# Optimization experiments

Measured on AMD Instinct MI355X. Metric: run time of the kernel, lower is better.

Reference implementation:

```python
import jax, jax.numpy as jnp
import numpy as np

VOCAB = 32000; D_MODEL = 768; N_LAYERS = 4
D_STATE = 16; D_CONV = 4; EXPAND = 2
D_INNER = EXPAND * D_MODEL                 # 1536
DT_RANK = (D_MODEL + 15) // 16             # 48
BATCH = 2; SEQ = 1024


def setup_inputs():
    key = jax.random.key(0)
    ks = jax.random.split(key, 10)
    def nrm(k, shape, scale=0.02):
        return (jax.random.normal(k, shape) * scale).astype(jnp.float32)
    inp = {}
    inp['tokens'] = jax.random.randint(ks[0], (BATCH, SEQ), 0, VOCAB)
    inp['embedding'] = nrm(ks[1], (VOCAB, D_MODEL))
    inp['head_bias'] = jnp.zeros((VOCAB,), jnp.float32)
    inp['ln_g'] = jnp.ones((N_LAYERS, D_MODEL), jnp.float32)
    inp['ln_b'] = jnp.zeros((N_LAYERS, D_MODEL), jnp.float32)
    inp['W_in'] = nrm(ks[2], (N_LAYERS, 2 * D_INNER, D_MODEL))
    inp['conv_w'] = nrm(ks[3], (N_LAYERS, D_INNER, 1, D_CONV), 0.1)
    inp['conv_b'] = jnp.zeros((N_LAYERS, D_INNER), jnp.float32)
    inp['W_xproj'] = nrm(ks[4], (N_LAYERS, DT_RANK + 2 * D_STATE, D_INNER))
    inp['W_dt'] = nrm(ks[5], (N_LAYERS, D_INNER, DT_RANK), 0.1)
    inp['b_dt'] = nrm(ks[6], (N_LAYERS, D_INNER), 0.5)
    # S4D-real init: A_n = n for n in 1..d_state
    inp['A_log'] = jnp.broadcast_to(jnp.log(jnp.arange(1, D_STATE + 1, dtype=jnp.float32)), (N_LAYERS, D_INNER, D_STATE)).copy()
    inp['D_ssm'] = jnp.ones((N_LAYERS, D_INNER), jnp.float32)
    inp['W_out'] = nrm(ks[7], (N_LAYERS, D_MODEL, D_INNER))
    inp['norm_g'] = jnp.ones((D_MODEL,), jnp.float32)
    inp['norm_b'] = jnp.zeros((D_MODEL,), jnp.float32)
    return inp


def _ln(x, g, b):
    m = jnp.mean(x, axis=-1, keepdims=True)
    v = jnp.var(x, axis=-1, keepdims=True)
    return (x - m) * jax.lax.rsqrt(v + 1e-5) * g + b


def _mamba(x, W_in, conv_w, conv_b, W_xproj, W_dt, b_dt, A_log, D_ssm, W_out):
    # x: (S, B, D_MODEL)
    xz = jnp.einsum('sbd,ed->sbe', x, W_in)           # (S, B, 2*D_INNER)
    xc, z = jnp.split(xz, 2, axis=-1)
    # depthwise causal conv along sequence
    xt = jnp.transpose(xc, (1, 2, 0))                  # (B, C, S)
    xt = jax.lax.conv_general_dilated(xt, conv_w, (1,), [(D_CONV - 1, 0)],
                                      dimension_numbers=('NCH', 'OIH', 'NCH'),
                                      feature_group_count=D_INNER)
    xt = xt + conv_b[None, :, None]
    xc = jax.nn.silu(jnp.transpose(xt, (2, 0, 1)))     # (S, B, C)
    xdb = jnp.einsum('sbc,ec->sbe', xc, W_xproj)       # (S, B, DT_RANK+2N)
    dt_r = xdb[..., :DT_RANK]
    Bm = xdb[..., DT_RANK:DT_RANK + D_STATE]
    Cm = xdb[..., DT_RANK + D_STATE:]
    dt = jax.nn.softplus(jnp.einsum('sbr,cr->sbc', dt_r, W_dt) + b_dt)
    A = -jnp.exp(A_log)                                # (C, N)

    def step(h, t):
        dt_t, B_t, C_t, x_t = t                        # (B,C),(B,N),(B,N),(B,C)
        dA = jnp.exp(dt_t[..., None] * A)              # (B, C, N)
        h = h * dA + (dt_t * x_t)[..., None] * B_t[:, None, :]
        y = jnp.einsum('bcn,bn->bc', h, C_t)
        return h, y

    h0 = jnp.zeros((x.shape[1], D_INNER, D_STATE), x.dtype)
    _, ys = jax.lax.scan(step, h0, (dt, Bm, Cm, xc))   # ys: (S, B, C)
    y = (ys + D_ssm * xc) * jax.nn.silu(z)
    return jnp.einsum('sbc,dc->sbd', y, W_out)


def reference(tokens, embedding, head_bias, ln_g, ln_b, W_in, conv_w, conv_b, W_xproj, W_dt, b_dt, A_log, D_ssm, W_out, norm_g, norm_b):
    x = embedding[tokens.T]                            # (S, B, D)
    for i in range(N_LAYERS):
        x = x + _mamba(_ln(x, ln_g[i], ln_b[i]), W_in[i], conv_w[i], conv_b[i],
                       W_xproj[i], W_dt[i], b_dt[i], A_log[i], D_ssm[i], W_out[i])
    x = _ln(x, norm_g, norm_b)
    logits = jnp.einsum('sbd,vd->sbv', x, embedding) + head_bias  # tied head
    return jnp.transpose(logits, (1, 0, 2))            # (B, S, VOCAB)
```

## Files before the change

### kernel.cpp

```cpp
#include <hip/hip_runtime.h>
#include <hip/hip_bf16.h>
#include <cstdint>
#include <cstddef>

#define SEQ_LEN 1024
#define NBATCH  2
#define MROWS   2048
#define DMODEL  768
#define DINNER  1536
#define DTRANK  48
#define DSTATE  16
#define NLAYERS 4
#define NVOCAB  32000
#define XPROJ_N 80
#define NCHUNK  16
#define CHUNK   64
#define GROUPS  (NBATCH * DINNER)
#define SCANW   (GROUPS * DSTATE)
#define XSPLIT  8

typedef __attribute__((ext_vector_type(4))) float f32x4;
typedef __attribute__((ext_vector_type(8))) short s16x8;
using bf16 = __hip_bfloat16;

__device__ __forceinline__ float b2f(bf16 v){ return __bfloat162float(v); }
__device__ __forceinline__ bf16  f2b(float v){ return __float2bfloat16(v); }
__device__ __forceinline__ short f2bs(float v){
  return (short)__builtin_bit_cast(unsigned short, __float2bfloat16(v));
}

__device__ __forceinline__ void glds16(const ushort* g, ushort* l) {
  __builtin_amdgcn_global_load_lds(
      (const __attribute__((address_space(1))) void*)g,
      (__attribute__((address_space(3))) void*)l,
      16, 0, 0);
}

#define CVT_E0 6144000
#define CVT_E1 (CVT_E0 + 2359296)
#define CVT_E2 (CVT_E1 + 1179648)
#define CVT_E3 (CVT_E2 + 122880)
#define CVT_E4 (CVT_E3 + 73728)
__global__ __launch_bounds__(256) void k_cvt5(
    const float* __restrict__ s0, const float* __restrict__ s1,
    const float* __restrict__ s2, const float* __restrict__ s3,
    const float* __restrict__ s4,
    ushort* __restrict__ d0, ushort* __restrict__ d1,
    ushort* __restrict__ d2, ushort* __restrict__ d3,
    ushort* __restrict__ d4)
{
  int i = blockIdx.x * 256 + threadIdx.x;
  const float* s; ushort* d; int base;
  if      (i < CVT_E0) { s = s0; d = d0; base = 0; }
  else if (i < CVT_E1) { s = s1; d = d1; base = CVT_E0; }
  else if (i < CVT_E2) { s = s2; d = d2; base = CVT_E1; }
  else if (i < CVT_E3) { s = s3; d = d3; base = CVT_E2; }
  else if (i < CVT_E4) { s = s4; d = d4; base = CVT_E3; }
  else return;
  int li = i - base;
  f32x4 v = *(const f32x4*)(s + (size_t)li * 4);
  ushort4 o;
  o.x = (ushort)f2bs(v[0]); o.y = (ushort)f2bs(v[1]);
  o.z = (ushort)f2bs(v[2]); o.w = (ushort)f2bs(v[3]);
  *(ushort4*)(d + (size_t)li * 4) = o;
}

__global__ __launch_bounds__(256) void k_xsum(const float* __restrict__ p,
    ushort* __restrict__ out, int n4) {
  int i = blockIdx.x * 256 + threadIdx.x;
  if (i >= n4) return;
  f32x4 s = {};
#pragma unroll
  for (int z = 0; z < XSPLIT; z++) {
    f32x4 v = *(const f32x4*)(p + (size_t)z * (MROWS * XPROJ_N) + (size_t)i * 4);
    s[0] += v[0]; s[1] += v[1]; s[2] += v[2]; s[3] += v[3];
  }
  ushort4 o;
  o.x = (ushort)f2bs(s[0]); o.y = (ushort)f2bs(s[1]);
  o.z = (ushort)f2bs(s[2]); o.w = (ushort)f2bs(s[3]);
  *(ushort4*)(out + (size_t)i * 4) = o;
}

__device__ __forceinline__ void ln_rows(const float v0[3], int t,
    const float* __restrict__ g, const float* __restrict__ b,
    bf16* __restrict__ outrow) {
  float s = 0.f, s2 = 0.f;
#pragma unroll
  for (int j = 0; j < 3; j++) { s += v0[j]; s2 += v0[j] * v0[j]; }
#pragma unroll
  for (int o = 32; o >= 1; o >>= 1) { s += __shfl_xor(s, o); s2 += __shfl_xor(s2, o); }
  __shared__ float red[8];
  int wave = t >> 6;
  if ((t & 63) == 0) { red[wave] = s; red[4 + wave] = s2; }
  __syncthreads();
  s  = red[0] + red[1] + red[2] + red[3];
  s2 = red[4] + red[5] + red[6] + red[7];
  float mean = s * (1.f / DMODEL);
  float var  = s2 * (1.f / DMODEL) - mean * mean;
  float rstd = rsqrtf(var + 1e-5f);
#pragma unroll
  for (int j = 0; j < 3; j++) {
    int d = t + j * 256;
    outrow[d] = f2b((v0[j] - mean) * rstd * g[d] + b[d]);
  }
}

__global__ __launch_bounds__(256) void k_ln(const float* __restrict__ x,
    bf16* __restrict__ out, const float* __restrict__ g, const float* __restrict__ b) {
  int m = blockIdx.x;
  const float* row = x + (size_t)m * DMODEL;
  int t = threadIdx.x;
  float v0[3];
#pragma unroll
  for (int j = 0; j < 3; j++) v0[j] = row[t + j * 256];
  ln_rows(v0, t, g, b, out + (size_t)m * DMODEL);
}

__global__ __launch_bounds__(256) void k_embed_ln(const int* __restrict__ tok,
    const float* __restrict__ emb, float* __restrict__ x,
    bf16* __restrict__ out, const float* __restrict__ g, const float* __restrict__ b) {
  int m = blockIdx.x;
  const float* row = emb + (size_t)tok[m] * DMODEL;
  int t = threadIdx.x;
  float v0[3];
#pragma unroll
  for (int j = 0; j < 3; j++) {
    v0[j] = row[t + j * 256];
    x[(size_t)m * DMODEL + t + j * 256] = v0[j];
  }
  ln_rows(v0, t, g, b, out + (size_t)m * DMODEL);
}

template<bool HAS_BIAS, int OMODE>
__global__ __launch_bounds__(512, 4) void k_gemm128(
    const ushort* __restrict__ A, int lda,
    const ushort* __restrict__ B, int ldb,
    void* __restrict__ C, int ldc,
    const float* __restrict__ bias,
    int M, int N, int K)
{
  __shared__ ushort As[2][128 * 32];
  __shared__ ushort Bs[2][128 * 32];
  const int t = threadIdx.x;
  const int lane = t & 63;
  const int wave = t >> 6;
  const int tile_m = blockIdx.x * 128;
  const int tile_n = blockIdx.y * 128;
  const int kper = K / gridDim.z;
  const int kb = blockIdx.z * kper;
  const int ke = kb + kper;
  const int wr = (wave >> 1) * 32;
  const int wc = (wave & 1) * 64;

  f32x4 acc[2][4] = {};

  const int sr = wave * 16 + (lane >> 2);
  const int sc = (lane & 3) * 8;
  const ushort* gA = A + (size_t)(tile_m + sr) * lda + sc + kb;
  const ushort* gB = B + (size_t)(tile_n + sr) * ldb + sc + kb;

  const int fr = lane & 15;
  const int kk = (lane >> 4) * 8;

  auto stage = [&](int bb) {
    glds16(gA, &As[bb][wave * 512]);
    glds16(gB, &Bs[bb][wave * 512]);
    gA += 32; gB += 32;
  };

  stage(0);
  int cur = 0;

  for (int k0 = kb; k0 < ke; k0 += 32) {
    if (k0 + 32 < ke) {
      stage(cur ^ 1);
      asm volatile("s_waitcnt vmcnt(2)" ::: "memory");
    } else {
      asm volatile("s_waitcnt vmcnt(0)" ::: "memory");
    }
    __builtin_amdgcn_s_barrier();

    s16x8 a[2], b[4];
#pragma unroll
    for (int m = 0; m < 2; m++)
      a[m] = *(const s16x8*)&As[cur][(wr + m * 16 + fr) * 32 + kk];
#pragma unroll
    for (int n = 0; n < 4; n++)
      b[n] = *(const s16x8*)&Bs[cur][(wc + n * 16 + fr) * 32 + kk];
#pragma unroll
    for (int m = 0; m < 2; m++)
#pragma unroll
      for (int n = 0; n < 4; n++)
        acc[m][n] = __builtin_amdgcn_mfma_f32_16x16x32_bf16(a[m], b[n], acc[m][n], 0, 0, 0);

    __builtin_amdgcn_s_barrier();
    cur ^= 1;
  }

  const int rq = (lane >> 4) * 4;
#pragma unroll
  for (int m = 0; m < 2; m++)
#pragma unroll
    for (int n = 0; n < 4; n++) {
      int colg = tile_n + wc + n * 16 + fr;
      float bv = HAS_BIAS ? bias[colg] : 0.f;
#pragma unroll
      for (int r = 0; r < 4; r++) {
        int rowg = tile_m + wr + m * 16 + rq + r;
        size_t idx = (size_t)rowg * ldc + colg;
        float v = acc[m][n][r] + bv;
        if constexpr (OMODE == 0) ((float*)C)[idx] = v;
        else if constexpr (OMODE == 1) atomicAdd((float*)C + idx, v);
        else ((bf16*)C)[idx] = f2b(v);
      }
    }
}

template<int MODE>
__global__ __launch_bounds__(256) void k_gemm(
    const ushort* __restrict__ A, int lda,
    const ushort* __restrict__ W, int ldw,
    void* __restrict__ Cout, int ldc,
    int M, int N, int K,
    const float* __restrict__ bias,
    const bf16* __restrict__ xcb,
    bf16* __restrict__ dtxp)
{
  __shared__ ushort As[64][40];
  __shared__ ushort Ws[64][40];
  const int tile_m = blockIdx.x * 64;
  const int tile_n = blockIdx.y * 64;
  const int t = threadIdx.x;
  const int lane = t & 63;
  const int wave = t >> 6;
  const int wr = (wave >> 1) * 32;
  const int wc = (wave & 1) * 32;
  f32x4 acc[2][2] = {};

  const int kper = ((K + gridDim.z - 1) / gridDim.z + 31) & ~31;
  const int kb = blockIdx.z * kper;
  int ke = kb + kper; if (ke > K) ke = K;

  const int srow = t >> 2;
  const int scol = (t & 3) * 8;

  for (int k0 = kb; k0 < ke; k0 += 32) {
    {
      int gm = tile_m + srow, gk = k0 + scol;
      s16x8 v = {};
      if (gm < M) {
        if (gk + 8 <= K) v = *(const s16x8*)(A + (size_t)gm * lda + gk);
        else {
#pragma unroll
          for (int j = 0; j < 8; j++) if (gk + j < K) v[j] = (short)A[(size_t)gm * lda + gk + j];
        }
      }
      *(s16x8*)&As[srow][scol] = v;
    }
    {
      int gn = tile_n + srow, gk = k0 + scol;
      s16x8 v = {};
      if (gn < N) {
        if (gk + 8 <= K) v = *(const s16x8*)(W + (size_t)gn * ldw + gk);
        else {
#pragma unroll
          for (int j = 0; j < 8; j++) if (gk + j < K) v[j] = (short)W[(size_t)gn * ldw + gk + j];
        }
      }
      *(s16x8*)&Ws[srow][scol] = v;
    }
    __syncthreads();
    const int kk = (lane >> 4) * 8;
    const int fr = lane & 15;
    s16x8 a0 = *(const s16x8*)&As[wr + fr][kk];
    s16x8 a1 = *(const s16x8*)&As[wr + 16 + fr][kk];
    s16x8 b0 = *(const s16x8*)&Ws[wc + fr][kk];
    s16x8 b1 = *(const s16x8*)&Ws[wc + 16 + fr][kk];
    acc[0][0] = __builtin_amdgcn_mfma_f32_16x16x32_bf16(a0, b0, acc[0][0], 0, 0, 0);
    acc[0][1] = __builtin_amdgcn_mfma_f32_16x16x32_bf16(a0, b1, acc[0][1], 0, 0, 0);
    acc[1][0] = __builtin_amdgcn_mfma_f32_16x16x32_bf16(a1, b0, acc[1][0], 0, 0, 0);
    acc[1][1] = __builtin_amdgcn_mfma_f32_16x16x32_bf16(a1, b1, acc[1][1], 0, 0, 0);
    __syncthreads();
  }

  const int fr = lane & 15;
  const int rq = (lane >> 4) * 4;
#pragma unroll
  for (int i = 0; i < 2; i++)
#pragma unroll
    for (int j = 0; j < 2; j++) {
      int colg = tile_n + wc + j * 16 + fr;
#pragma unroll
      for (int r = 0; r < 4; r++) {
        int rowg = tile_m + wr + i * 16 + rq + r;
        if (rowg < M && colg < N) {
          float v = acc[i][j][r];
          size_t idx = (size_t)rowg * ldc + colg;
          if constexpr (MODE == 0) {
            ((bf16*)Cout)[idx] = f2b(v);
          } else if constexpr (MODE == 2) {
            v += bias[colg];
            float sp = (v > 20.f) ? v : log1pf(__expf(v));
            ((float*)Cout)[idx] = sp;
            dtxp[idx] = f2b(sp * b2f(xcb[idx]));
          } else {
            ((float*)Cout)[(size_t)blockIdx.z * (MROWS * XPROJ_N) + idx] = v;
          }
        }
      }
    }
}

__global__ __launch_bounds__(256) void k_conv(const bf16* __restrict__ xz,
    const float* __restrict__ w, const float* __restrict__ cb,
    bf16* __restrict__ xcb) {
  int id = blockIdx.x * 256 + threadIdx.x;
  int m = id / DINNER, c = id - m * DINNER;
  int s = m & (SEQ_LEN - 1);
  float acc = cb[c];
#pragma unroll
  for (int k = 0; k < 4; k++) {
    int sp = s - 3 + k;
    if (sp >= 0) acc += w[c * 4 + k] * b2f(xz[(size_t)(m - 3 + k) * (2 * DINNER) + c]);
  }
  float sil = acc / (1.f + __expf(-acc));
  xcb[id] = f2b(sil);
}

__global__ __launch_bounds__(256) void k_scan1(const float* __restrict__ dt,
    const bf16* __restrict__ dtx, const bf16* __restrict__ xdb,
    const float* __restrict__ A_log, float* __restrict__ aprod,
    float* __restrict__ hend) {
  int gid = blockIdx.x * 256 + threadIdx.x;
  int n  = gid & 15;
  int t2 = gid >> 4;
  int j  = t2 / GROUPS;
  int cb = t2 - j * GROUPS;
  int c  = cb % DINNER;
  int b  = cb / DINNER;
  float Acn = -__expf(A_log[c * DSTATE + n]);
  float h = 0.f, ap = 1.f;
  int mbase = b * SEQ_LEN + j * CHUNK;
#pragma unroll 4
  for (int s = 0; s < CHUNK; s++) {
    int m = mbase + s;
    float dtv = dt[(size_t)m * DINNER + c];
    float dxv = b2f(dtx[(size_t)m * DINNER + c]);
    float Bv  = b2f(xdb[(size_t)m * XPROJ_N + DTRANK + n]);
    float dA  = __expf(dtv * Acn);
    h = h * dA + dxv * Bv;
    ap *= dA;
  }
  aprod[gid] = ap;
  hend[gid]  = h;
}

__global__ __launch_bounds__(256) void k_scan2(const float* __restrict__ aprod,
    const float* __restrict__ hend, float* __restrict__ hin) {
  int idx = blockIdx.x * 256 + threadIdx.x;
  float h = 0.f;
#pragma unroll
  for (int j = 0; j < NCHUNK; j++) {
    hin[(size_t)j * SCANW + idx] = h;
    h = aprod[(size_t)j * SCANW + idx] * h + hend[(size_t)j * SCANW + idx];
  }
}

__global__ __launch_bounds__(256) void k_scan3(const float* __restrict__ dt,
    const bf16* __restrict__ dtx, const bf16* __restrict__ xdb,
    const float* __restrict__ A_log, const float* __restrict__ hin,
    bf16* __restrict__ y) {
  int gid = blockIdx.x * 256 + threadIdx.x;
  int n  = gid & 15;
  int t2 = gid >> 4;
  int j  = t2 / GROUPS;
  int cb = t2 - j * GROUPS;
  int c  = cb % DINNER;
  int b  = cb / DINNER;
  float Acn = -__expf(A_log[c * DSTATE + n]);
  float h = hin[gid];
  int mbase = b * SEQ_LEN + j * CHUNK;
#pragma unroll 2
  for (int s = 0; s < CHUNK; s++) {
    int m = mbase + s;
    float dtv = dt[(size_t)m * DINNER + c];
    float dxv = b2f(dtx[(size_t)m * DINNER + c]);
    float Bv  = b2f(xdb[(size_t)m * XPROJ_N + DTRANK + n]);
    float Cv  = b2f(xdb[(size_t)m * XPROJ_N + DTRANK + DSTATE + n]);
    float dA  = __expf(dtv * Acn);
    h = h * dA + dxv * Bv;
    float p = h * Cv;
    p += __shfl_xor(p, 8);
    p += __shfl_xor(p, 4);
    p += __shfl_xor(p, 2);
    p += __shfl_xor(p, 1);
    if (n == 0) y[(size_t)m * DINNER + c] = f2b(p);
  }
}

__global__ __launch_bounds__(256) void k_ycomb(const bf16* __restrict__ y,
    const bf16* __restrict__ xcb, const bf16* __restrict__ xz,
    const float* __restrict__ D_ssm, bf16* __restrict__ ybf) {
  int id = blockIdx.x * 256 + threadIdx.x;
  int m = id / DINNER, c = id - m * DINNER;
  float z = b2f(xz[(size_t)m * (2 * DINNER) + DINNER + c]);
  float sil = z / (1.f + __expf(-z));
  float v = (b2f(y[id]) + D_ssm[c] * b2f(xcb[id])) * sil;
  ybf[id] = f2b(v);
}

extern "C" void kernel_launch(void* const* d_in, const int* in_sizes, int n_in,
                              void* d_out, int out_size, void* d_ws, size_t ws_size,
                              hipStream_t stream) {
  const int*   tokens    = (const int*)  d_in[0];
  const float* embedding = (const float*)d_in[1];
  const float* head_bias = (const float*)d_in[2];
  const float* ln_g      = (const float*)d_in[3];
  const float* ln_b      = (const float*)d_in[4];
  const float* W_in      = (const float*)d_in[5];
  const float* conv_w    = (const float*)d_in[6];
  const float* conv_b    = (const float*)d_in[7];
  const float* W_xproj   = (const float*)d_in[8];
  const float* W_dt      = (const float*)d_in[9];
  const float* b_dt      = (const float*)d_in[10];
  const float* A_log     = (const float*)d_in[11];
  const float* D_ssm     = (const float*)d_in[12];
  const float* W_out     = (const float*)d_in[13];
  const float* norm_g    = (const float*)d_in[14];
  const float* norm_b    = (const float*)d_in[15];
  float* out = (float*)d_out;

  char* ws = (char*)d_ws;
  size_t off = 0;
  auto alloc = [&](size_t bytes) -> char* {
    char* p = ws + off;
    off = (off + bytes + 255) & ~(size_t)255;
    return p;
  };
  float*  x     = (float*) alloc((size_t)MROWS * DMODEL * 4);
  bf16*   xln   = (bf16*)  alloc((size_t)MROWS * DMODEL * 2);
  bf16*   xz    = (bf16*)  alloc((size_t)MROWS * 2 * DINNER * 2);
  bf16*   xcb   = (bf16*)  alloc((size_t)MROWS * DINNER * 2);
  bf16*   xdb   = (bf16*)  alloc((size_t)MROWS * XPROJ_N * 2);
  float*  xdbp  = (float*) alloc((size_t)XSPLIT * MROWS * XPROJ_N * 4);
  float*  dtf   = (float*) alloc((size_t)MROWS * DINNER * 4);
  bf16*   dtx   = (bf16*)  alloc((size_t)MROWS * DINNER * 2);
  bf16*   yraw  = (bf16*)  alloc((size_t)MROWS * DINNER * 2);
  bf16*   ybf   = (bf16*)  alloc((size_t)MROWS * DINNER * 2);
  float*  aprod = (float*) alloc((size_t)SCANW * NCHUNK * 4);
  float*  hend  = (float*) alloc((size_t)SCANW * NCHUNK * 4);
  float*  hin   = (float*) alloc((size_t)SCANW * NCHUNK * 4);
  ushort* ebf   = (ushort*)alloc((size_t)NVOCAB * DMODEL * 2);
  ushort* winb  = (ushort*)alloc((size_t)NLAYERS * 2 * DINNER * DMODEL * 2);
  ushort* wxpb  = (ushort*)alloc((size_t)NLAYERS * XPROJ_N * DINNER * 2);
  ushort* wdtb  = (ushort*)alloc((size_t)NLAYERS * DINNER * DTRANK * 2);
  ushort* woutb = (ushort*)alloc((size_t)NLAYERS * DMODEL * DINNER * 2);
  (void)ws_size; (void)in_sizes; (void)n_in; (void)out_size;

  k_cvt5<<<(CVT_E4 + 255) / 256, 256, 0, stream>>>(
      embedding, W_in, W_out, W_xproj, W_dt,
      ebf, winb, woutb, wxpb, wdtb);

  k_embed_ln<<<MROWS, 256, 0, stream>>>(tokens, embedding, x, xln, ln_g, ln_b);

  const int XDBN4 = MROWS * XPROJ_N / 4;

  for (int L = 0; L < NLAYERS; L++) {
    if (L > 0)
      k_ln<<<MROWS, 256, 0, stream>>>(x, xln, ln_g + L * DMODEL, ln_b + L * DMODEL);

    k_gemm128<false, 2><<<dim3(MROWS / 128, (2 * DINNER) / 128), 512, 0, stream>>>(
        (const ushort*)xln, DMODEL,
        winb + (size_t)L * 2 * DINNER * DMODEL, DMODEL,
        (void*)xz, 2 * DINNER, nullptr, MROWS, 2 * DINNER, DMODEL);

    k_conv<<<MROWS * DINNER / 256, 256, 0, stream>>>(
        xz, conv_w + (size_t)L * DINNER * 4, conv_b + (size_t)L * DINNER, xcb);

    k_gemm<3><<<dim3(MROWS / 64, 2, XSPLIT), 256, 0, stream>>>(
        (const ushort*)xcb, DINNER,
        wxpb + (size_t)L * XPROJ_N * DINNER, DINNER,
        (void*)xdbp, XPROJ_N, MROWS, XPROJ_N, DINNER,
        nullptr, nullptr, nullptr);
    k_xsum<<<(XDBN4 + 255) / 256, 256, 0, stream>>>(xdbp, (ushort*)xdb, XDBN4);

    k_gemm<2><<<dim3(MROWS / 64, DINNER / 64), 256, 0, stream>>>(
        (const ushort*)xdb, XPROJ_N,
        wdtb + (size_t)L * DINNER * DTRANK, DTRANK,
        (void*)dtf, DINNER, MROWS, DINNER, DTRANK,
        b_dt + (size_t)L * DINNER, xcb, dtx);

    const float* Al = A_log + (size_t)L * DINNER * DSTATE;
    k_scan1<<<SCANW * NCHUNK / 256, 256, 0, stream>>>(dtf, dtx, xdb, Al, aprod, hend);
    k_scan2<<<SCANW / 256, 256, 0, stream>>>(aprod, hend, hin);
    k_scan3<<<SCANW * NCHUNK / 256, 256, 0, stream>>>(dtf, dtx, xdb, Al, hin, yraw);

    k_ycomb<<<MROWS * DINNER / 256, 256, 0, stream>>>(
        yraw, xcb, xz, D_ssm + (size_t)L * DINNER, ybf);

    k_gemm128<false, 1><<<dim3(MROWS / 128, DMODEL / 128, 4), 512, 0, stream>>>(
        (const ushort*)ybf, DINNER,
        woutb + (size_t)L * DMODEL * DINNER, DINNER,
        (void*)x, DMODEL, nullptr, MROWS, DMODEL, DINNER);
  }

  k_ln<<<MROWS, 256, 0, stream>>>(x, xln, norm_g, norm_b);

  k_gemm128<true, 0><<<dim3(MROWS / 128, NVOCAB / 128), 512, 0, stream>>>(
      (const ushort*)xln, DMODEL,
      ebf, DMODEL,
      out, NVOCAB, head_bias, MROWS, NVOCAB, DMODEL);
}
```

Before: 980.9 us.

## Fuse three-pass chunked scan into one kernel and enlarge LM-head GEMM tile

The chunked selective scan's three kernels (per-chunk reduce, cross-chunk prefix, per-chunk apply) become one kernel. Each block handles one (batch, channel) pair, and the cross-chunk carry is resolved in shared memory, so the aprod/hend/hin global buffers and two launches per layer go away. The scan inputs are also read twice within the same block, which may improve cache reuse. The LM-head GEMM moves to a new 256x128-tile kernel with double-buffered direct-to-LDS loads, meant to cut repeated embedding-matrix reads. The trade-off is higher register and LDS use per block, and a serial prefix over 16 chunks inside each block.

```diff
diff --git a/kernel.cpp b/kernel.cpp
--- a/kernel.cpp
+++ b/kernel.cpp
@@ -216,6 +216,86 @@
     }
 }
 
+template<bool HAS_BIAS>
+__global__ __launch_bounds__(512, 4) void k_gemmbig(
+    const ushort* __restrict__ A, int lda,
+    const ushort* __restrict__ B, int ldb,
+    float* __restrict__ C, int ldc,
+    const float* __restrict__ bias,
+    int M, int N, int K)
+{
+  __shared__ ushort As[2][256 * 32];
+  __shared__ ushort Bs[2][128 * 32];
+  const int t = threadIdx.x;
+  const int lane = t & 63;
+  const int wave = t >> 6;
+  const int tile_m = blockIdx.x * 256;
+  const int tile_n = blockIdx.y * 128;
+  const int wr = (wave >> 1) * 64;
+  const int wc = (wave & 1) * 64;
+
+  f32x4 acc[4][4] = {};
+
+  const int sr = wave * 16 + (lane >> 2);
+  const int sc = (lane & 3) * 8;
+  const ushort* gA0 = A + (size_t)(tile_m + sr) * lda + sc;
+  const ushort* gA1 = A + (size_t)(tile_m + 128 + sr) * lda + sc;
+  const ushort* gB  = B + (size_t)(tile_n + sr) * ldb + sc;
+
+  const int fr = lane & 15;
+  const int kk = (lane >> 4) * 8;
+
+  auto stage = [&](int bb) {
+    glds16(gA0, &As[bb][wave * 512]);
+    glds16(gA1, &As[bb][4096 + wave * 512]);
+    glds16(gB,  &Bs[bb][wave * 512]);
+    gA0 += 32; gA1 += 32; gB += 32;
+  };
+
+  stage(0);
+  int cur = 0;
+
+  for (int k0 = 0; k0 < K; k0 += 32) {
+    if (k0 + 32 < K) {
+      stage(cur ^ 1);
+      asm volatile("s_waitcnt vmcnt(3)" ::: "memory");
+    } else {
+      asm volatile("s_waitcnt vmcnt(0)" ::: "memory");
+    }
+    __builtin_amdgcn_s_barrier();
+
+    s16x8 a[4], b[4];
+#pragma unroll
+    for (int m = 0; m < 4; m++)
+      a[m] = *(const s16x8*)&As[cur][(wr + m * 16 + fr) * 32 + kk];
+#pragma unroll
+    for (int n = 0; n < 4; n++)
+      b[n] = *(const s16x8*)&Bs[cur][(wc + n * 16 + fr) * 32 + kk];
+#pragma unroll
+    for (int m = 0; m < 4; m++)
+#pragma unroll
+      for (int n = 0; n < 4; n++)
+        acc[m][n] = __builtin_amdgcn_mfma_f32_16x16x32_bf16(a[m], b[n], acc[m][n], 0, 0, 0);
+
+    __builtin_amdgcn_s_barrier();
+    cur ^= 1;
+  }
+
+  const int rq = (lane >> 4) * 4;
+#pragma unroll
+  for (int m = 0; m < 4; m++)
+#pragma unroll
+    for (int n = 0; n < 4; n++) {
+      int colg = tile_n + wc + n * 16 + fr;
+      float bv = HAS_BIAS ? bias[colg] : 0.f;
+#pragma unroll
+      for (int r = 0; r < 4; r++) {
+        int rowg = tile_m + wr + m * 16 + rq + r;
+        C[(size_t)rowg * ldc + colg] = acc[m][n][r] + bv;
+      }
+    }
+}
+
 template<int MODE>
 __global__ __launch_bounds__(256) void k_gemm(
     const ushort* __restrict__ A, int lda,
@@ -327,20 +407,17 @@
   xcb[id] = f2b(sil);
 }
 
-__global__ __launch_bounds__(256) void k_scan1(const float* __restrict__ dt,
+__global__ __launch_bounds__(256) void k_scan(const float* __restrict__ dt,
     const bf16* __restrict__ dtx, const bf16* __restrict__ xdb,
-    const float* __restrict__ A_log, float* __restrict__ aprod,
-    float* __restrict__ hend) {
-  int gid = blockIdx.x * 256 + threadIdx.x;
-  int n  = gid & 15;
-  int t2 = gid >> 4;
-  int j  = t2 / GROUPS;
-  int cb = t2 - j * GROUPS;
-  int c  = cb % DINNER;
-  int b  = cb / DINNER;
+    const float* __restrict__ A_log, bf16* __restrict__ y) {
+  int cb = blockIdx.x;
+  int c = cb % DINNER, b = cb / DINNER;
+  int t = threadIdx.x;
+  int n = t & 15, j = t >> 4;
   float Acn = -__expf(A_log[c * DSTATE + n]);
+  int mbase = b * SEQ_LEN + j * CHUNK;
+
   float h = 0.f, ap = 1.f;
-  int mbase = b * SEQ_LEN + j * CHUNK;
 #pragma unroll 4
   for (int s = 0; s < CHUNK; s++) {
     int m = mbase + s;
@@ -351,35 +428,23 @@
     h = h * dA + dxv * Bv;
     ap *= dA;
   }
-  aprod[gid] = ap;
-  hend[gid]  = h;
-}
-
-__global__ __launch_bounds__(256) void k_scan2(const float* __restrict__ aprod,
-    const float* __restrict__ hend, float* __restrict__ hin) {
-  int idx = blockIdx.x * 256 + threadIdx.x;
-  float h = 0.f;
-#pragma unroll
-  for (int j = 0; j < NCHUNK; j++) {
-    hin[(size_t)j * SCANW + idx] = h;
-    h = aprod[(size_t)j * SCANW + idx] * h + hend[(size_t)j * SCANW + idx];
-  }
-}
-
-__global__ __launch_bounds__(256) void k_scan3(const float* __restrict__ dt,
-    const bf16* __restrict__ dtx, const bf16* __restrict__ xdb,
-    const float* __restrict__ A_log, const float* __restrict__ hin,
-    bf16* __restrict__ y) {
-  int gid = blockIdx.x * 256 + threadIdx.x;
-  int n  = gid & 15;
-  int t2 = gid >> 4;
-  int j  = t2 / GROUPS;
-  int cb = t2 - j * GROUPS;
-  int c  = cb % DINNER;
-  int b  = cb / DINNER;
-  float Acn = -__expf(A_log[c * DSTATE + n]);
-  float h = hin[gid];
-  int mbase = b * SEQ_LEN + j * CHUNK;
+
+  __shared__ float Ap[NCHUNK][DSTATE + 1];
+  __shared__ float He[NCHUNK][DSTATE + 1];
+  __shared__ float Hin[NCHUNK][DSTATE + 1];
+  Ap[j][n] = ap; He[j][n] = h;
+  __syncthreads();
+  if (t < DSTATE) {
+    float hh = 0.f;
+#pragma unroll
+    for (int jj = 0; jj < NCHUNK; jj++) {
+      Hin[jj][t] = hh;
+      hh = Ap[jj][t] * hh + He[jj][t];
+    }
+  }
+  __syncthreads();
+
+  h = Hin[j][n];
 #pragma unroll 2
   for (int s = 0; s < CHUNK; s++) {
     int m = mbase + s;
@@ -447,9 +512,6 @@
   bf16*   dtx   = (bf16*)  alloc((size_t)MROWS * DINNER * 2);
   bf16*   yraw  = (bf16*)  alloc((size_t)MROWS * DINNER * 2);
   bf16*   ybf   = (bf16*)  alloc((size_t)MROWS * DINNER * 2);
-  float*  aprod = (float*) alloc((size_t)SCANW * NCHUNK * 4);
-  float*  hend  = (float*) alloc((size_t)SCANW * NCHUNK * 4);
-  float*  hin   = (float*) alloc((size_t)SCANW * NCHUNK * 4);
   ushort* ebf   = (ushort*)alloc((size_t)NVOCAB * DMODEL * 2);
   ushort* winb  = (ushort*)alloc((size_t)NLAYERS * 2 * DINNER * DMODEL * 2);
   ushort* wxpb  = (ushort*)alloc((size_t)NLAYERS * XPROJ_N * DINNER * 2);
@@ -490,10 +552,8 @@
         (void*)dtf, DINNER, MROWS, DINNER, DTRANK,
         b_dt + (size_t)L * DINNER, xcb, dtx);
 
-    const float* Al = A_log + (size_t)L * DINNER * DSTATE;
-    k_scan1<<<SCANW * NCHUNK / 256, 256, 0, stream>>>(dtf, dtx, xdb, Al, aprod, hend);
-    k_scan2<<<SCANW / 256, 256, 0, stream>>>(aprod, hend, hin);
-    k_scan3<<<SCANW * NCHUNK / 256, 256, 0, stream>>>(dtf, dtx, xdb, Al, hin, yraw);
+    k_scan<<<GROUPS, 256, 0, stream>>>(
+        dtf, dtx, xdb, A_log + (size_t)L * DINNER * DSTATE, yraw);
 
     k_ycomb<<<MROWS * DINNER / 256, 256, 0, stream>>>(
         yraw, xcb, xz, D_ssm + (size_t)L * DINNER, ybf);
@@ -506,7 +566,7 @@
 
   k_ln<<<MROWS, 256, 0, stream>>>(x, xln, norm_g, norm_b);
 
-  k_gemm128<true, 0><<<dim3(MROWS / 128, NVOCAB / 128), 512, 0, stream>>>(
+  k_gemmbig<true><<<dim3(MROWS / 256, NVOCAB / 128), 512, 0, stream>>>(
       (const ushort*)xln, DMODEL,
       ebf, DMODEL,
       out, NVOCAB, head_bias, MROWS, NVOCAB, DMODEL);
```

Result: slower. 1.093 ms (+11.4%).
